# Performance work log

Hardware: AMD Instinct MI355X
Metric: run time of the kernel (lower is better)

The kernel has to match this reference:

```python
import jax, jax.numpy as jnp
import numpy as np

NU = 30000   # n_users
NI = 15000   # n_items
D = 64       # embed_dim (== layer widths)
R = 5        # ratingClass == ratingSocial
NU5 = NU * R
NI5 = NI * R
NADJ = NU + NI5
NNZ_S = 1_200_000
NNZ_A = 840_000


def _spmm(rows, cols, vals, x, n_rows):
    # sparse (COO) matrix @ dense: out[r] = sum_e vals[e] * x[cols[e]] for rows[e]==r
    return jax.ops.segment_sum(vals[:, None] * x[cols], rows, num_segments=n_rows)


def _prelu(x, alpha):
    return jnp.where(x >= 0, x, alpha[0] * x)


def setup_inputs() -> dict:
    key = jax.random.key(0)
    ks = jax.random.split(key, 12)
    sc = lambda fan: 1.0 / np.sqrt(fan)
    return {
        "user_emb": 0.1 * jax.random.normal(ks[0], (NU5, D), jnp.float32),
        "item_emb": 0.1 * jax.random.normal(ks[1], (NI5, D), jnp.float32),
        "w_r1_w": sc(2 * D) * jax.random.normal(ks[2], (D, 2 * D), jnp.float32),
        "w_r1_b": jnp.zeros((D,), jnp.float32),
        "social_w1": sc(D) * jax.random.normal(ks[3], (D, D), jnp.float32),
        "user_w1": sc(D) * jax.random.normal(ks[4], (D, D), jnp.float32),
        "item_w1": sc(D) * jax.random.normal(ks[5], (D, D), jnp.float32),
        "alpha": jnp.full((1,), 0.25, jnp.float32),  # PReLU default init
        "social_vals": jax.random.uniform(ks[6], (NNZ_S,), jnp.float32) / 8.0,
        "adj_vals": jax.random.uniform(ks[7], (NNZ_A,), jnp.float32) / 8.0,
        "social_rows": jax.random.randint(ks[8], (NNZ_S,), 0, NU5, jnp.int32),
        "social_cols": jax.random.randint(ks[9], (NNZ_S,), 0, NU5, jnp.int32),
        "adj_rows": jax.random.randint(ks[10], (NNZ_A,), 0, NADJ, jnp.int32),
        "adj_cols": jax.random.randint(ks[11], (NNZ_A,), 0, NADJ, jnp.int32),
    }


def reference(user_emb, item_emb, w_r1_w, w_r1_b, social_w1, user_w1, item_w1,
              alpha, social_vals, adj_vals, social_rows, social_cols,
              adj_rows, adj_cols):
    # --- getSocialEmbedding ---
    e0 = _prelu(_spmm(social_rows, social_cols, social_vals, user_emb, NU5), alpha)
    e1 = _prelu(_spmm(social_rows, social_cols, social_vals, e0 @ social_w1, NU5), alpha)
    u_multi = jnp.concatenate([e0, e1], axis=1)            # (NU5, 128)
    u_social = u_multi.reshape(NU, R, 2 * D).sum(axis=1) / 4.0  # (NU, 128)

    # --- forward ---
    u = u_social @ w_r1_w.T + w_r1_b                        # Linear(128 -> 64)
    ego = jnp.concatenate([u, item_emb], axis=0)            # (NADJ, 64)
    emb = _prelu(_spmm(adj_rows, adj_cols, adj_vals, ego, NADJ), alpha)
    au0, ai0 = emb[:NU], emb[NU:]
    ego1 = jnp.concatenate([au0 @ user_w1, ai0 @ item_w1], axis=0)
    emb1 = _prelu(_spmm(adj_rows, adj_cols, adj_vals, ego1, NADJ), alpha)
    au1, ai1 = emb1[:NU], emb1[NU:]

    user_embedding = jnp.concatenate([au0, au1], axis=1)    # (NU, 128)
    item_multi = jnp.concatenate([ai0, ai1], axis=1)        # (NI5, 128)
    item_embedding = item_multi.reshape(NI, R, 2 * D).sum(axis=1) / 5.0
    return (user_embedding, item_embedding)
```

## Files before the change

kernel.cpp:

```cpp
#include <hip/hip_runtime.h>
#include <hip/hip_bf16.h>

#define NUu 30000
#define NIi 15000
#define DD 64
#define RR 5
#define NU5 150000
#define NI5 75000
#define NADJ 105000
#define NNZ_S 1200000
#define NNZ_A 840000

#define SCAN_TPB 256
#define SCAN_ELEMS 8
#define SCAN_CHUNK (SCAN_TPB * SCAN_ELEMS)

__global__ void csr_count(const int* __restrict__ rows, int nnz, int* __restrict__ counts) {
    int e = blockIdx.x * blockDim.x + threadIdx.x;
    if (e < nnz) atomicAdd(&counts[rows[e]], 1);
}

__global__ void scan_partial(const int* __restrict__ counts, int n,
                             int* __restrict__ ptr, int* __restrict__ blocksums) {
    __shared__ int sh[SCAN_TPB];
    int base = blockIdx.x * SCAN_CHUNK;
    int t = threadIdx.x;
    int loc[SCAN_ELEMS];
    int s = 0;
#pragma unroll
    for (int i = 0; i < SCAN_ELEMS; ++i) {
        int idx = base + t * SCAN_ELEMS + i;
        int v = (idx < n) ? counts[idx] : 0;
        loc[i] = s;
        s += v;
    }
    sh[t] = s;
    __syncthreads();
    for (int off = 1; off < SCAN_TPB; off <<= 1) {
        int v = (t >= off) ? sh[t - off] : 0;
        __syncthreads();
        sh[t] += v;
        __syncthreads();
    }
    int texcl = (t == 0) ? 0 : sh[t - 1];
    if (t == SCAN_TPB - 1) blocksums[blockIdx.x] = sh[t];
#pragma unroll
    for (int i = 0; i < SCAN_ELEMS; ++i) {
        int idx = base + t * SCAN_ELEMS + i;
        if (idx < n) ptr[idx] = texcl + loc[i];
    }
}

__global__ void scan_blocksums(int* __restrict__ blocksums, int nblocks) {
    __shared__ int sh[SCAN_TPB];
    int t = threadIdx.x;
    int v = (t < nblocks) ? blocksums[t] : 0;
    sh[t] = v;
    __syncthreads();
    for (int off = 1; off < SCAN_TPB; off <<= 1) {
        int u = (t >= off) ? sh[t - off] : 0;
        __syncthreads();
        sh[t] += u;
        __syncthreads();
    }
    int excl = (t == 0) ? 0 : sh[t - 1];
    if (t < nblocks) blocksums[t] = excl;
}

__global__ void scan_add(int* __restrict__ ptr, int* __restrict__ cursor, int n, int nnz,
                         const int* __restrict__ blocksums) {
    int i = blockIdx.x * blockDim.x + threadIdx.x;
    if (i < n) {
        int v = ptr[i] + blocksums[i / SCAN_CHUNK];
        ptr[i] = v;
        cursor[i] = v;
    }
    if (i == 0) ptr[n] = nnz;
}

__global__ void csr_fill(const int* __restrict__ rows, const int* __restrict__ cols,
                         const float* __restrict__ vals, int nnz, int* __restrict__ cursor,
                         int2* __restrict__ ecv) {
    int e = blockIdx.x * blockDim.x + threadIdx.x;
    if (e >= nnz) return;
    int p = atomicAdd(&cursor[rows[e]], 1);
    ecv[p] = make_int2(cols[e], __float_as_int(vals[e]));
}

template <bool SPLIT>
__global__ void spmm_csr(const int* __restrict__ ptr, const int2* __restrict__ ecv,
                         const float* __restrict__ x, const float* __restrict__ x2,
                         float* __restrict__ out, int nrows) {
    int w = (blockIdx.x * blockDim.x + threadIdx.x) >> 6;
    int lane = threadIdx.x & 63;
    if (w >= nrows) return;
    int beg = ptr[w], end = ptr[w + 1];
    float a0 = 0.f, a1 = 0.f, a2 = 0.f, a3 = 0.f;
    int j = beg;
    for (; j + 3 < end; j += 4) {
        int2 e0 = ecv[j], e1 = ecv[j + 1], e2 = ecv[j + 2], e3 = ecv[j + 3];
        const float *p0, *p1, *p2, *p3;
        if (SPLIT) {
            p0 = (e0.x < NUu) ? x + (size_t)e0.x * DD : x2 + (size_t)(e0.x - NUu) * DD;
            p1 = (e1.x < NUu) ? x + (size_t)e1.x * DD : x2 + (size_t)(e1.x - NUu) * DD;
            p2 = (e2.x < NUu) ? x + (size_t)e2.x * DD : x2 + (size_t)(e2.x - NUu) * DD;
            p3 = (e3.x < NUu) ? x + (size_t)e3.x * DD : x2 + (size_t)(e3.x - NUu) * DD;
        } else {
            p0 = x + (size_t)e0.x * DD;
            p1 = x + (size_t)e1.x * DD;
            p2 = x + (size_t)e2.x * DD;
            p3 = x + (size_t)e3.x * DD;
        }
        a0 += __int_as_float(e0.y) * p0[lane];
        a1 += __int_as_float(e1.y) * p1[lane];
        a2 += __int_as_float(e2.y) * p2[lane];
        a3 += __int_as_float(e3.y) * p3[lane];
    }
    for (; j < end; ++j) {
        int2 e0 = ecv[j];
        const float* p0;
        if (SPLIT)
            p0 = (e0.x < NUu) ? x + (size_t)e0.x * DD : x2 + (size_t)(e0.x - NUu) * DD;
        else
            p0 = x + (size_t)e0.x * DD;
        a0 += __int_as_float(e0.y) * p0[lane];
    }
    out[(size_t)w * DD + lane] = (a0 + a1) + (a2 + a3);
}

__global__ void spmm_atomic(const int* __restrict__ rows, const int* __restrict__ cols,
                            const float* __restrict__ vals, const float* __restrict__ x,
                            float* __restrict__ out, int nnz) {
    int tid = blockIdx.x * blockDim.x + threadIdx.x;
    int e = tid >> 4;
    if (e >= nnz) return;
    int lc = (tid & 15) << 2;
    int r = rows[e];
    int c = cols[e];
    float v = vals[e];
    const float4 xv = *reinterpret_cast<const float4*>(x + (size_t)c * DD + lc);
    float* o = out + (size_t)r * DD + lc;
    unsafeAtomicAdd(o + 0, v * xv.x);
    unsafeAtomicAdd(o + 1, v * xv.y);
    unsafeAtomicAdd(o + 2, v * xv.z);
    unsafeAtomicAdd(o + 3, v * xv.w);
}

#define PRELU(v) ((v) >= 0.f ? (v) : alpha * (v))

__global__ void gemm64_prelu(const float* __restrict__ X, const float* __restrict__ W,
                             const float* __restrict__ alpha_p, float* __restrict__ Y,
                             int nrows) {
    __shared__ float4 Ws[64 * 16];
    int t = threadIdx.x;
    {
        const float4* Wv = (const float4*)W;
        for (int i = t; i < 1024; i += 256) Ws[i] = Wv[i];
    }
    __syncthreads();
    float alpha = alpha_p[0];
    int lane = t & 63;
    int g = t >> 6;
    int row = blockIdx.x * 64 + lane;
    if (row >= nrows) return;

    float xr[64];
    const float4* xp = (const float4*)(X + (size_t)row * DD);
#pragma unroll
    for (int i = 0; i < 16; ++i) {
        float4 v = xp[i];
        xr[4 * i + 0] = PRELU(v.x);
        xr[4 * i + 1] = PRELU(v.y);
        xr[4 * i + 2] = PRELU(v.z);
        xr[4 * i + 3] = PRELU(v.w);
    }
    float4 a0 = {0, 0, 0, 0}, a1 = a0, a2 = a0, a3 = a0;
#pragma unroll
    for (int k = 0; k < 64; ++k) {
        float xk = xr[k];
        const float4* wr = &Ws[k * 16 + g * 4];
        float4 w0 = wr[0], w1 = wr[1], w2 = wr[2], w3 = wr[3];
        a0.x += xk * w0.x; a0.y += xk * w0.y; a0.z += xk * w0.z; a0.w += xk * w0.w;
        a1.x += xk * w1.x; a1.y += xk * w1.y; a1.z += xk * w1.z; a1.w += xk * w1.w;
        a2.x += xk * w2.x; a2.y += xk * w2.y; a2.z += xk * w2.z; a2.w += xk * w2.w;
        a3.x += xk * w3.x; a3.y += xk * w3.y; a3.z += xk * w3.z; a3.w += xk * w3.w;
    }
    float4* yp = (float4*)(Y + (size_t)row * DD + g * 16);
    yp[0] = a0; yp[1] = a1; yp[2] = a2; yp[3] = a3;
}

__global__ void fuse_u(const float* __restrict__ raw0, const float* __restrict__ raw1,
                       const float* __restrict__ w_r1_w, const float* __restrict__ w_r1_b,
                       const float* __restrict__ alpha_p, float* __restrict__ uout) {
    __shared__ float Wl[128 * 68];
    int t = threadIdx.x;
    for (int i = t; i < 8192; i += 256) {
        int j = i >> 7, k = i & 127;
        Wl[k * 68 + j] = w_r1_w[i];
    }
    __syncthreads();
    float alpha = alpha_p[0];
    int lane = t & 63;
    int g = t >> 6;
    int row = blockIdx.x * 64 + lane;
    if (row >= NUu) return;

    const float4* bp = (const float4*)(w_r1_b + g * 16);
    float4 a0 = bp[0], a1 = bp[1], a2 = bp[2], a3 = bp[3];
    float xr[64];

    const float4* rp = (const float4*)(raw0 + (size_t)row * RR * DD);
#pragma unroll
    for (int i = 0; i < 16; ++i) {
        float sx = 0.f, sy = 0.f, sz = 0.f, sw = 0.f;
#pragma unroll
        for (int r = 0; r < RR; ++r) {
            float4 v = rp[r * 16 + i];
            sx += PRELU(v.x); sy += PRELU(v.y); sz += PRELU(v.z); sw += PRELU(v.w);
        }
        xr[4 * i + 0] = sx * 0.25f;
        xr[4 * i + 1] = sy * 0.25f;
        xr[4 * i + 2] = sz * 0.25f;
        xr[4 * i + 3] = sw * 0.25f;
    }
#pragma unroll
    for (int k = 0; k < 64; ++k) {
        float xk = xr[k];
        const float4* wr = (const float4*)(Wl + k * 68 + g * 16);
        float4 w0 = wr[0], w1 = wr[1], w2 = wr[2], w3 = wr[3];
        a0.x += xk * w0.x; a0.y += xk * w0.y; a0.z += xk * w0.z; a0.w += xk * w0.w;
        a1.x += xk * w1.x; a1.y += xk * w1.y; a1.z += xk * w1.z; a1.w += xk * w1.w;
        a2.x += xk * w2.x; a2.y += xk * w2.y; a2.z += xk * w2.z; a2.w += xk * w2.w;
        a3.x += xk * w3.x; a3.y += xk * w3.y; a3.z += xk * w3.z; a3.w += xk * w3.w;
    }
    rp = (const float4*)(raw1 + (size_t)row * RR * DD);
#pragma unroll
    for (int i = 0; i < 16; ++i) {
        float sx = 0.f, sy = 0.f, sz = 0.f, sw = 0.f;
#pragma unroll
        for (int r = 0; r < RR; ++r) {
            float4 v = rp[r * 16 + i];
            sx += PRELU(v.x); sy += PRELU(v.y); sz += PRELU(v.z); sw += PRELU(v.w);
        }
        xr[4 * i + 0] = sx * 0.25f;
        xr[4 * i + 1] = sy * 0.25f;
        xr[4 * i + 2] = sz * 0.25f;
        xr[4 * i + 3] = sw * 0.25f;
    }
#pragma unroll
    for (int k = 0; k < 64; ++k) {
        float xk = xr[k];
        const float4* wr = (const float4*)(Wl + (64 + k) * 68 + g * 16);
        float4 w0 = wr[0], w1 = wr[1], w2 = wr[2], w3 = wr[3];
        a0.x += xk * w0.x; a0.y += xk * w0.y; a0.z += xk * w0.z; a0.w += xk * w0.w;
        a1.x += xk * w1.x; a1.y += xk * w1.y; a1.z += xk * w1.z; a1.w += xk * w1.w;
        a2.x += xk * w2.x; a2.y += xk * w2.y; a2.z += xk * w2.z; a2.w += xk * w2.w;
        a3.x += xk * w3.x; a3.y += xk * w3.y; a3.z += xk * w3.z; a3.w += xk * w3.w;
    }
    float4* yp = (float4*)(uout + (size_t)row * DD + g * 16);
    yp[0] = a0; yp[1] = a1; yp[2] = a2; yp[3] = a3;
}

__global__ void fuse_ego1(const float* __restrict__ embraw, const float* __restrict__ Wu,
                          const float* __restrict__ Wi, const float* __restrict__ alpha_p,
                          float* __restrict__ ego1) {
    __shared__ float4 Ws[2 * 64 * 16];
    int t = threadIdx.x;
    {
        const float4* Wv = (const float4*)Wu;
        const float4* Wv2 = (const float4*)Wi;
        for (int i = t; i < 1024; i += 256) {
            Ws[i] = Wv[i];
            Ws[1024 + i] = Wv2[i];
        }
    }
    __syncthreads();
    float alpha = alpha_p[0];
    int lane = t & 63;
    int g = t >> 6;
    int row = blockIdx.x * 64 + lane;
    if (row >= NADJ) return;
    const float4* Wb = (row < NUu) ? Ws : Ws + 1024;

    float xr[64];
    const float4* xp = (const float4*)(embraw + (size_t)row * DD);
#pragma unroll
    for (int i = 0; i < 16; ++i) {
        float4 v = xp[i];
        xr[4 * i + 0] = PRELU(v.x);
        xr[4 * i + 1] = PRELU(v.y);
        xr[4 * i + 2] = PRELU(v.z);
        xr[4 * i + 3] = PRELU(v.w);
    }
    float4 a0 = {0, 0, 0, 0}, a1 = a0, a2 = a0, a3 = a0;
#pragma unroll
    for (int k = 0; k < 64; ++k) {
        float xk = xr[k];
        const float4* wr = &Wb[k * 16 + g * 4];
        float4 w0 = wr[0], w1 = wr[1], w2 = wr[2], w3 = wr[3];
        a0.x += xk * w0.x; a0.y += xk * w0.y; a0.z += xk * w0.z; a0.w += xk * w0.w;
        a1.x += xk * w1.x; a1.y += xk * w1.y; a1.z += xk * w1.z; a1.w += xk * w1.w;
        a2.x += xk * w2.x; a2.y += xk * w2.y; a2.z += xk * w2.z; a2.w += xk * w2.w;
        a3.x += xk * w3.x; a3.y += xk * w3.y; a3.z += xk * w3.z; a3.w += xk * w3.w;
    }
    float4* yp = (float4*)(ego1 + (size_t)row * DD + g * 16);
    yp[0] = a0; yp[1] = a1; yp[2] = a2; yp[3] = a3;
}

__global__ void out_combined(const float* __restrict__ embraw, const float* __restrict__ emb1raw,
                             const float* __restrict__ alpha_p, float* __restrict__ outp) {
    float alpha = alpha_p[0];
    int i = blockIdx.x * blockDim.x + threadIdx.x;
    if (i < NUu * DD) {
        int row = i >> 6, c = i & 63;
        float a = embraw[i];
        a = PRELU(a);
        float b = emb1raw[i];
        b = PRELU(b);
        outp[(size_t)row * 128 + c] = a;
        outp[(size_t)row * 128 + 64 + c] = b;
    } else {
        int i2 = i - NUu * DD;
        if (i2 >= NIi * DD) return;
        int row = i2 >> 6, c = i2 & 63;
        float s0 = 0.f, s1 = 0.f;
#pragma unroll
        for (int r = 0; r < RR; ++r) {
            size_t idx = ((size_t)NUu + (size_t)row * RR + r) * DD + c;
            float a = embraw[idx];
            s0 += PRELU(a);
            float b = emb1raw[idx];
            s1 += PRELU(b);
        }
        size_t obase = (size_t)NUu * 128 + (size_t)row * 128 + c;
        outp[obase] = s0 / 5.0f;
        outp[obase + 64] = s1 / 5.0f;
    }
}

static void build_csr(const int* rows, const int* cols, const float* vals, int nnz, int nrows,
                      int* ptr, int* cur, int2* ecv, int* bsums, hipStream_t stream) {
    hipMemsetAsync(cur, 0, (size_t)nrows * sizeof(int), stream);
    csr_count<<<(nnz + 255) / 256, 256, 0, stream>>>(rows, nnz, cur);
    int nblocks = (nrows + SCAN_CHUNK - 1) / SCAN_CHUNK;
    scan_partial<<<nblocks, SCAN_TPB, 0, stream>>>(cur, nrows, ptr, bsums);
    scan_blocksums<<<1, SCAN_TPB, 0, stream>>>(bsums, nblocks);
    scan_add<<<(nrows + 255) / 256, 256, 0, stream>>>(ptr, cur, nrows, nnz, bsums);
    csr_fill<<<(nnz + 255) / 256, 256, 0, stream>>>(rows, cols, vals, nnz, cur, ecv);
}

extern "C" void kernel_launch(void* const* d_in, const int* in_sizes, int n_in,
                              void* d_out, int out_size, void* d_ws, size_t ws_size,
                              hipStream_t stream) {
    const float* user_emb  = (const float*)d_in[0];
    const float* item_emb  = (const float*)d_in[1];
    const float* w_r1_w    = (const float*)d_in[2];
    const float* w_r1_b    = (const float*)d_in[3];
    const float* social_w1 = (const float*)d_in[4];
    const float* user_w1   = (const float*)d_in[5];
    const float* item_w1   = (const float*)d_in[6];
    const float* alpha     = (const float*)d_in[7];
    const float* social_vals = (const float*)d_in[8];
    const float* adj_vals    = (const float*)d_in[9];
    const int* social_rows = (const int*)d_in[10];
    const int* social_cols = (const int*)d_in[11];
    const int* adj_rows    = (const int*)d_in[12];
    const int* adj_cols    = (const int*)d_in[13];
    float* out = (float*)d_out;

    float* A  = (float*)d_ws;
    float* B  = A + (size_t)NU5 * DD;
    float* C  = B + (size_t)NU5 * DD;
    float* Dm = C + (size_t)NU5 * DD;
    int*  s_ptr = (int*)(Dm + (size_t)NADJ * DD);
    int*  s_cur = s_ptr + (NU5 + 2);
    int2* s_ecv = (int2*)(s_cur + NU5);
    int*  a_ptr = (int*)(s_ecv + NNZ_S);
    int*  a_cur = a_ptr + (NADJ + 2);
    int2* a_ecv = (int2*)(a_cur + NADJ);
    int*  bsums = (int*)(a_ecv + NNZ_A);
    size_t need = (size_t)((char*)(bsums + 128) - (char*)d_ws);

    if (ws_size >= need) {
        build_csr(social_rows, social_cols, social_vals, NNZ_S, NU5,
                  s_ptr, s_cur, s_ecv, bsums, stream);
        build_csr(adj_rows, adj_cols, adj_vals, NNZ_A, NADJ,
                  a_ptr, a_cur, a_ecv, bsums, stream);

        spmm_csr<false><<<(NU5 * 64 + 255) / 256, 256, 0, stream>>>(
            s_ptr, s_ecv, user_emb, nullptr, A, NU5);
        gemm64_prelu<<<(NU5 + 63) / 64, 256, 0, stream>>>(A, social_w1, alpha, B, NU5);
        spmm_csr<false><<<(NU5 * 64 + 255) / 256, 256, 0, stream>>>(
            s_ptr, s_ecv, B, nullptr, C, NU5);
        fuse_u<<<(NUu + 63) / 64, 256, 0, stream>>>(A, C, w_r1_w, w_r1_b, alpha, B);
        spmm_csr<true><<<(NADJ * 64 + 255) / 256, 256, 0, stream>>>(
            a_ptr, a_ecv, B, item_emb, Dm, NADJ);
        fuse_ego1<<<(NADJ + 63) / 64, 256, 0, stream>>>(Dm, user_w1, item_w1, alpha, A);
        spmm_csr<false><<<(NADJ * 64 + 255) / 256, 256, 0, stream>>>(
            a_ptr, a_ecv, A, nullptr, C, NADJ);
    } else {
        hipMemsetAsync(A, 0, (size_t)NU5 * DD * sizeof(float), stream);
        spmm_atomic<<<(NNZ_S * 16 + 255) / 256, 256, 0, stream>>>(
            social_rows, social_cols, social_vals, user_emb, A, NNZ_S);
        gemm64_prelu<<<(NU5 + 63) / 64, 256, 0, stream>>>(A, social_w1, alpha, B, NU5);
        hipMemsetAsync(C, 0, (size_t)NU5 * DD * sizeof(float), stream);
        spmm_atomic<<<(NNZ_S * 16 + 255) / 256, 256, 0, stream>>>(
            social_rows, social_cols, social_vals, B, C, NNZ_S);
        fuse_u<<<(NUu + 63) / 64, 256, 0, stream>>>(A, C, w_r1_w, w_r1_b, alpha, B);
        hipMemcpyAsync(B + (size_t)NUu * DD, item_emb, (size_t)NI5 * DD * sizeof(float),
                       hipMemcpyDeviceToDevice, stream);
        hipMemsetAsync(Dm, 0, (size_t)NADJ * DD * sizeof(float), stream);
        spmm_atomic<<<(NNZ_A * 16 + 255) / 256, 256, 0, stream>>>(
            adj_rows, adj_cols, adj_vals, B, Dm, NNZ_A);
        fuse_ego1<<<(NADJ + 63) / 64, 256, 0, stream>>>(Dm, user_w1, item_w1, alpha, A);
        hipMemsetAsync(C, 0, (size_t)NADJ * DD * sizeof(float), stream);
        spmm_atomic<<<(NNZ_A * 16 + 255) / 256, 256, 0, stream>>>(
            adj_rows, adj_cols, adj_vals, A, C, NNZ_A);
    }

    out_combined<<<((NUu + NIi) * DD + 255) / 256, 256, 0, stream>>>(Dm, C, alpha, out);
}
```

Baseline: 739.2 us.

## Build CSR via two-pass bucket partitioning to localize scatter writes

```diff
diff --git a/kernel.cpp b/kernel.cpp
--- a/kernel.cpp
+++ b/kernel.cpp
@@ -15,10 +15,12 @@
 #define SCAN_ELEMS 8
 #define SCAN_CHUNK (SCAN_TPB * SCAN_ELEMS)
 
-__global__ void csr_count(const int* __restrict__ rows, int nnz, int* __restrict__ counts) {
-    int e = blockIdx.x * blockDim.x + threadIdx.x;
-    if (e < nnz) atomicAdd(&counts[rows[e]], 1);
-}
+#define NBK 256
+#define CHUNK 2048
+#define CAP_S 10240
+#define CAP_A 5120
+#define NBUCK_S ((NU5 + 1023) >> 10)
+#define NBUCK_A ((NADJ + 511) >> 9)
 
 __global__ void scan_partial(const int* __restrict__ counts, int n,
                              int* __restrict__ ptr, int* __restrict__ blocksums) {
@@ -78,13 +80,78 @@
     if (i == 0) ptr[n] = nnz;
 }
 
-__global__ void csr_fill(const int* __restrict__ rows, const int* __restrict__ cols,
-                         const float* __restrict__ vals, int nnz, int* __restrict__ cursor,
-                         int2* __restrict__ ecv) {
-    int e = blockIdx.x * blockDim.x + threadIdx.x;
-    if (e >= nnz) return;
-    int p = atomicAdd(&cursor[rows[e]], 1);
-    ecv[p] = make_int2(cols[e], __float_as_int(vals[e]));
+template <int SH>
+__global__ __launch_bounds__(256) void partition_edges(
+    const int* __restrict__ rows, const int* __restrict__ cols,
+    const float* __restrict__ vals, int nnz, int* __restrict__ counts,
+    int* __restrict__ gcur, int4* __restrict__ part, int cap) {
+    __shared__ int4 stage[CHUNK];
+    __shared__ int hist[NBK], start[NBK], gbase[NBK], lcur[NBK];
+    int t = threadIdx.x;
+    int base = blockIdx.x * CHUNK;
+    int nrem = nnz - base;
+    int n = nrem < CHUNK ? nrem : CHUNK;
+    hist[t] = 0;
+    __syncthreads();
+    int r[8], c[8];
+    float v[8];
+#pragma unroll
+    for (int k = 0; k < 8; ++k) {
+        int li = t + k * 256;
+        if (li < n) {
+            int i = base + li;
+            r[k] = rows[i];
+            c[k] = cols[i];
+            v[k] = vals[i];
+            atomicAdd(&hist[r[k] >> SH], 1);
+            atomicAdd(&counts[r[k]], 1);
+        } else {
+            r[k] = -1;
+        }
+    }
+    __syncthreads();
+    int hv = hist[t];
+    start[t] = hv;
+    __syncthreads();
+    for (int off = 1; off < NBK; off <<= 1) {
+        int u = (t >= off) ? start[t - off] : 0;
+        __syncthreads();
+        start[t] += u;
+        __syncthreads();
+    }
+    int excl = start[t] - hv;
+    __syncthreads();
+    start[t] = excl;
+    lcur[t] = excl;
+    gbase[t] = (hv > 0) ? atomicAdd(&gcur[t], hv) : 0;
+    __syncthreads();
+#pragma unroll
+    for (int k = 0; k < 8; ++k) {
+        if (r[k] >= 0) {
+            int b = r[k] >> SH;
+            int p = atomicAdd(&lcur[b], 1);
+            stage[p] = make_int4(r[k], c[k], __float_as_int(v[k]), 0);
+        }
+    }
+    __syncthreads();
+    for (int j = t; j < n; j += 256) {
+        int4 e = stage[j];
+        int b = e.x >> SH;
+        part[(size_t)b * cap + gbase[b] + (j - start[b])] = e;
+    }
+}
+
+__global__ __launch_bounds__(256) void bucket_fill(
+    const int4* __restrict__ part, const int* __restrict__ gcur, int cap,
+    int* __restrict__ cursor, int2* __restrict__ ecv) {
+    int b = blockIdx.x;
+    int cnt = gcur[b];
+    const int4* seg = part + (size_t)b * cap;
+    for (int j = threadIdx.x; j < cnt; j += 256) {
+        int4 e = seg[j];
+        int p = atomicAdd(&cursor[e.x], 1);
+        ecv[p] = make_int2(e.y, e.z);
+    }
 }
 
 template <bool SPLIT>
@@ -338,17 +405,6 @@
     }
 }
 
-static void build_csr(const int* rows, const int* cols, const float* vals, int nnz, int nrows,
-                      int* ptr, int* cur, int2* ecv, int* bsums, hipStream_t stream) {
-    hipMemsetAsync(cur, 0, (size_t)nrows * sizeof(int), stream);
-    csr_count<<<(nnz + 255) / 256, 256, 0, stream>>>(rows, nnz, cur);
-    int nblocks = (nrows + SCAN_CHUNK - 1) / SCAN_CHUNK;
-    scan_partial<<<nblocks, SCAN_TPB, 0, stream>>>(cur, nrows, ptr, bsums);
-    scan_blocksums<<<1, SCAN_TPB, 0, stream>>>(bsums, nblocks);
-    scan_add<<<(nrows + 255) / 256, 256, 0, stream>>>(ptr, cur, nrows, nnz, bsums);
-    csr_fill<<<(nnz + 255) / 256, 256, 0, stream>>>(rows, cols, vals, nnz, cur, ecv);
-}
-
 extern "C" void kernel_launch(void* const* d_in, const int* in_sizes, int n_in,
                               void* d_out, int out_size, void* d_ws, size_t ws_size,
                               hipStream_t stream) {
@@ -379,13 +435,34 @@
     int*  a_cur = a_ptr + (NADJ + 2);
     int2* a_ecv = (int2*)(a_cur + NADJ);
     int*  bsums = (int*)(a_ecv + NNZ_A);
-    size_t need = (size_t)((char*)(bsums + 128) - (char*)d_ws);
+    int*  gcur  = bsums + 128;
+    size_t need = (size_t)((char*)(gcur + NBK) - (char*)d_ws);
+    int4* part = (int4*)A;
 
     if (ws_size >= need) {
-        build_csr(social_rows, social_cols, social_vals, NNZ_S, NU5,
-                  s_ptr, s_cur, s_ecv, bsums, stream);
-        build_csr(adj_rows, adj_cols, adj_vals, NNZ_A, NADJ,
-                  a_ptr, a_cur, a_ecv, bsums, stream);
+        hipMemsetAsync(s_cur, 0, (size_t)NU5 * sizeof(int), stream);
+        hipMemsetAsync(gcur, 0, NBK * sizeof(int), stream);
+        partition_edges<10><<<(NNZ_S + CHUNK - 1) / CHUNK, 256, 0, stream>>>(
+            social_rows, social_cols, social_vals, NNZ_S, s_cur, gcur, part, CAP_S);
+        {
+            int nblocks = (NU5 + SCAN_CHUNK - 1) / SCAN_CHUNK;
+            scan_partial<<<nblocks, SCAN_TPB, 0, stream>>>(s_cur, NU5, s_ptr, bsums);
+            scan_blocksums<<<1, SCAN_TPB, 0, stream>>>(bsums, nblocks);
+            scan_add<<<(NU5 + 255) / 256, 256, 0, stream>>>(s_ptr, s_cur, NU5, NNZ_S, bsums);
+        }
+        bucket_fill<<<NBUCK_S, 256, 0, stream>>>(part, gcur, CAP_S, s_cur, s_ecv);
+
+        hipMemsetAsync(a_cur, 0, (size_t)NADJ * sizeof(int), stream);
+        hipMemsetAsync(gcur, 0, NBK * sizeof(int), stream);
+        partition_edges<9><<<(NNZ_A + CHUNK - 1) / CHUNK, 256, 0, stream>>>(
+            adj_rows, adj_cols, adj_vals, NNZ_A, a_cur, gcur, part, CAP_A);
+        {
+            int nblocks = (NADJ + SCAN_CHUNK - 1) / SCAN_CHUNK;
+            scan_partial<<<nblocks, SCAN_TPB, 0, stream>>>(a_cur, NADJ, a_ptr, bsums);
+            scan_blocksums<<<1, SCAN_TPB, 0, stream>>>(bsums, nblocks);
+            scan_add<<<(NADJ + 255) / 256, 256, 0, stream>>>(a_ptr, a_cur, NADJ, NNZ_A, bsums);
+        }
+        bucket_fill<<<NBUCK_A, 256, 0, stream>>>(part, gcur, CAP_A, a_cur, a_ecv);
 
         spmm_csr<false><<<(NU5 * 64 + 255) / 256, 256, 0, stream>>>(
             s_ptr, s_ecv, user_emb, nullptr, A, NU5);
```

Result: faster. 700.2 us (-5.3%).
